# Kernel tuning notes

Hardware: AMD Instinct MI355X
Metric: run time of the kernel (lower is better)

Reference implementation:

```python
import jax, jax.numpy as jnp
import numpy as np

EPS = 1e-5

def layernorm(x, g, b):
    mu = jnp.mean(x, axis=-1, keepdims=True)
    var = jnp.mean(jnp.square(x - mu), axis=-1, keepdims=True)
    return (x - mu) * jax.lax.rsqrt(var + EPS) * g + b

def setup_inputs() -> dict:
    key = jax.random.key(0)
    B, T, C, H = 4, 2048, 1024, 16
    hs = C // H
    ks = jax.random.split(key, 16)
    s_in = 0.02
    return {
        "x": jax.random.normal(ks[0], (B, T, C), jnp.float32),
        "ln1_g": jnp.ones((C,), jnp.float32),
        "ln1_b": jnp.zeros((C,), jnp.float32),
        "Wq": jax.random.normal(ks[1], (H, C, hs), jnp.float32) * s_in,
        "Wk": jax.random.normal(ks[2], (H, C, hs), jnp.float32) * s_in,
        "Wv": jax.random.normal(ks[3], (H, C, hs), jnp.float32) * s_in,
        "Wo": jax.random.normal(ks[4], (C, C), jnp.float32) * s_in,
        "bo": jnp.zeros((C,), jnp.float32),
        "ln2_g": jnp.ones((C,), jnp.float32),
        "ln2_b": jnp.zeros((C,), jnp.float32),
        "W1": jax.random.normal(ks[5], (C, 4 * C), jnp.float32) * s_in,
        "b1": jnp.zeros((4 * C,), jnp.float32),
        "W2": jax.random.normal(ks[6], (4 * C, C), jnp.float32) * s_in,
        "b2": jnp.zeros((C,), jnp.float32),
    }

def reference(x, ln1_g, ln1_b, Wq, Wk, Wv, Wo, bo, ln2_g, ln2_b, W1, b1, W2, b2):
    B, T, C = x.shape
    H, _, hs = Wq.shape
    # --- multi-head causal self-attention on LN1(x) ---
    h = layernorm(x, ln1_g, ln1_b)
    q = jnp.einsum('btc,hcs->bhts', h, Wq)
    k = jnp.einsum('btc,hcs->bhts', h, Wk)
    v = jnp.einsum('btc,hcs->bhts', h, Wv)
    scores = jnp.einsum('bhqs,bhks->bhqk', q, k) * (hs ** -0.5)
    causal = jnp.tril(jnp.ones((T, T), bool))
    scores = jnp.where(causal, scores, -jnp.inf)
    attn = jax.nn.softmax(scores, axis=-1)  # dropout p=0 -> identity
    out = jnp.einsum('bhqk,bhks->bhqs', attn, v)
    out = out.transpose(0, 2, 1, 3).reshape(B, T, H * hs)  # concat heads
    x = x + out @ Wo + bo
    # --- feed-forward on LN2(x) ---
    h2 = layernorm(x, ln2_g, ln2_b)
    ff = jax.nn.relu(h2 @ W1 + b1) @ W2 + b2
    return x + ff
```

## Files before the change

### kernel.cpp

```cpp
#include <hip/hip_runtime.h>
#include <math.h>

#define B_  4
#define T_  2048
#define C_  1024
#define H_  16
#define HS_ 64
#define BT_ (B_*T_)
#define F_  (4*C_)
#define N3_ (3*C_)

typedef unsigned short ushort_t;
typedef __attribute__((ext_vector_type(4))) unsigned short us4;
typedef __attribute__((ext_vector_type(8))) unsigned short us8;
typedef __attribute__((ext_vector_type(4))) float f32x4;
typedef __attribute__((ext_vector_type(8))) __bf16 bf16x8;

template<bool V> struct bool_c { static constexpr bool value = V; };

__device__ __forceinline__ float bf2f(ushort_t u) {
    union { unsigned int i; float f; } c; c.i = ((unsigned int)u) << 16; return c.f;
}
__device__ __forceinline__ ushort_t f2bf(float f) {
    union { __bf16 b; ushort_t u; } c; c.b = (__bf16)f; return c.u;
}

#define GLB_(p) ((const __attribute__((address_space(1))) unsigned int*)(size_t)(p))
#define LDS_(p) ((__attribute__((address_space(3))) unsigned int*)(unsigned int)(size_t)(p))
__device__ __forceinline__ void gload16(const void* g, void* l) {
    __builtin_amdgcn_global_load_lds(GLB_(g), LDS_(l), 16, 0, 0);
}

template<int N> __device__ __forceinline__ void vm_wait() {
    if constexpr (N >= 8)      asm volatile("s_waitcnt vmcnt(8)" ::: "memory");
    else if constexpr (N == 6) asm volatile("s_waitcnt vmcnt(6)" ::: "memory");
    else if constexpr (N == 4) asm volatile("s_waitcnt vmcnt(4)" ::: "memory");
    else if constexpr (N == 3) asm volatile("s_waitcnt vmcnt(3)" ::: "memory");
    else if constexpr (N == 2) asm volatile("s_waitcnt vmcnt(2)" ::: "memory");
    else                       asm volatile("s_waitcnt vmcnt(0)" ::: "memory");
}

__global__ __launch_bounds__(256) void repack_qkv_k(
    const float* __restrict__ Wq, const float* __restrict__ Wk,
    const float* __restrict__ Wv, ushort_t* __restrict__ WtB)
{
    __shared__ float tile[64][65];
    int bid = blockIdx.x;
    int p  = bid >> 8;
    int h  = (bid >> 4) & 15;
    int c0 = (bid & 15) * 64;
    const float* W = (p == 0) ? Wq : ((p == 1) ? Wk : Wv);
    int t = threadIdx.x;
    int cl = t >> 2, seg = (t & 3) * 16;
    const float* src = W + ((size_t)h * C_ + c0 + cl) * HS_ + seg;
#pragma unroll
    for (int i = 0; i < 4; i++) {
        float4 v = *(const float4*)(src + i * 4);
        tile[cl][seg + i*4 + 0] = v.x; tile[cl][seg + i*4 + 1] = v.y;
        tile[cl][seg + i*4 + 2] = v.z; tile[cl][seg + i*4 + 3] = v.w;
    }
    __syncthreads();
    int sl = t >> 2;
    int n = p * C_ + h * HS_ + sl;
    ushort_t* dst = WtB + (size_t)n * C_ + c0 + seg;
    us8 o0, o1;
#pragma unroll
    for (int e = 0; e < 8; e++) { o0[e] = f2bf(tile[seg + e][sl]); o1[e] = f2bf(tile[seg + 8 + e][sl]); }
    *(us8*)dst = o0; *(us8*)(dst + 8) = o1;
}

__global__ __launch_bounds__(256) void transpose_k(
    const float* __restrict__ in, ushort_t* __restrict__ out, int K, int N)
{
    __shared__ float tile[64][65];
    int n0 = blockIdx.x * 64, k0 = blockIdx.y * 64;
    int t = threadIdx.x;
    int kl = t >> 2, seg = (t & 3) * 16;
    const float* src = in + (size_t)(k0 + kl) * N + n0 + seg;
#pragma unroll
    for (int i = 0; i < 4; i++) {
        float4 v = *(const float4*)(src + i * 4);
        tile[kl][seg + i*4 + 0] = v.x; tile[kl][seg + i*4 + 1] = v.y;
        tile[kl][seg + i*4 + 2] = v.z; tile[kl][seg + i*4 + 3] = v.w;
    }
    __syncthreads();
    int nl = t >> 2;
    ushort_t* dst = out + (size_t)(n0 + nl) * K + k0 + seg;
    us8 o0, o1;
#pragma unroll
    for (int e = 0; e < 8; e++) { o0[e] = f2bf(tile[seg + e][nl]); o1[e] = f2bf(tile[seg + 8 + e][nl]); }
    *(us8*)dst = o0; *(us8*)(dst + 8) = o1;
}

__global__ __launch_bounds__(256) void transv_k(
    const ushort_t* __restrict__ QKV, ushort_t* __restrict__ Vt)
{
    __shared__ ushort_t tl[64][72];
    int bid = blockIdx.x;
    int tt = bid & 31;
    int bh = bid >> 5;
    int b  = bh >> 4;
    int h  = bh & 15;
    int t = threadIdx.x;
    int r = t >> 2, sg = (t & 3) * 16;
    const ushort_t* src = QKV + (size_t)(b * T_ + tt * 64 + r) * N3_ + 2 * C_ + h * HS_ + sg;
    us8 a0 = *(const us8*)src;
    us8 a1 = *(const us8*)(src + 8);
#pragma unroll
    for (int e = 0; e < 8; e++) { tl[r][sg + e] = a0[e]; tl[r][sg + 8 + e] = a1[e]; }
    __syncthreads();
    ushort_t* dst = Vt + ((size_t)(b * H_ + h) * HS_ + r) * T_ + tt * 64 + sg;
    us8 o0, o1;
#pragma unroll
    for (int e = 0; e < 8; e++) { o0[e] = tl[sg + e][r]; o1[e] = tl[sg + 8 + e][r]; }
    *(us8*)dst = o0; *(us8*)(dst + 8) = o1;
}

template<int IN_BF16>
__global__ __launch_bounds__(256) void ln_k(
    const void* __restrict__ xv, const float* __restrict__ g,
    const float* __restrict__ b, ushort_t* __restrict__ out)
{
    int row = blockIdx.x;
    int t = threadIdx.x;
    float v[4];
    if (IN_BF16) {
        const ushort_t* xr = (const ushort_t*)xv + (size_t)row * C_;
        us4 u = *(const us4*)(xr + t * 4);
#pragma unroll
        for (int i = 0; i < 4; i++) v[i] = bf2f(u[i]);
    } else {
        const float* xr = (const float*)xv + (size_t)row * C_;
        float4 f = *(const float4*)(xr + t * 4);
        v[0] = f.x; v[1] = f.y; v[2] = f.z; v[3] = f.w;
    }
    float s  = v[0] + v[1] + v[2] + v[3];
    float ss = v[0]*v[0] + v[1]*v[1] + v[2]*v[2] + v[3]*v[3];
#pragma unroll
    for (int off = 32; off > 0; off >>= 1) {
        s  += __shfl_xor(s, off);
        ss += __shfl_xor(ss, off);
    }
    __shared__ float red[8];
    int wv = t >> 6;
    if ((t & 63) == 0) { red[wv*2] = s; red[wv*2+1] = ss; }
    __syncthreads();
    s  = red[0] + red[2] + red[4] + red[6];
    ss = red[1] + red[3] + red[5] + red[7];
    float mu  = s * (1.0f / C_);
    float var = ss * (1.0f / C_) - mu * mu;
    float rs  = rsqrtf(var + 1e-5f);
    float4 gv = *(const float4*)(g + t * 4);
    float4 bv = *(const float4*)(b + t * 4);
    us4 o;
    o[0] = f2bf((v[0] - mu) * rs * gv.x + bv.x);
    o[1] = f2bf((v[1] - mu) * rs * gv.y + bv.y);
    o[2] = f2bf((v[2] - mu) * rs * gv.z + bv.z);
    o[3] = f2bf((v[3] - mu) * rs * gv.w + bv.w);
    *(us4*)(out + (size_t)row * C_ + t * 4) = o;
}

template<int BM, int BN, int WM, int WN, int RELU, int BIAS, int RES_MODE, int OUT_BF16>
__global__ __launch_bounds__(WM * WN * 64) void mgemm8_k(
    const ushort_t* __restrict__ A, const ushort_t* __restrict__ Bw,
    const float* __restrict__ bias, const void* __restrict__ res,
    void* __restrict__ out, int M, int N, int K, int lda, int gx)
{
    constexpr int THREADS = WM * WN * 64;
    constexpr int MIa = BM / WM / 16;
    constexpr int MIb = BN / WN / 16;
    constexpr int A_INSTS = (BM * 64) / (16 * THREADS);
    constexpr int B_INSTS = (BN * 64) / (16 * THREADS);
    constexpr int UNIT = A_INSTS + B_INSTS;
    __shared__ ushort_t As[4 * BM * 32];
    __shared__ ushort_t Bs[4 * BN * 32];

    int tid = threadIdx.x;
    int l = tid & 63, w = tid >> 6;
    int wm = w / WN, wn = w % WN;
    int lin = blockIdx.x;
    int nwg = gridDim.x;
    int swz = (lin & 7) * (nwg >> 3) + (lin >> 3);
    int bx = swz % gx, by = swz / gx;
    int m0 = by * BM, n0 = bx * BN;
    const int nt = K >> 6;

    auto stageA = [&](int tile, int kh) {
        ushort_t* dst = As + ((tile & 1) * 2 + kh) * (BM * 32);
#pragma unroll
        for (int inst = 0; inst < A_INSTS; ++inst) {
            int slot = inst * THREADS + tid;
            int row = slot >> 2, q = slot & 3;
            const ushort_t* src = A + (size_t)(m0 + row) * lda + tile * 64 + kh * 32
                                  + ((q ^ ((row >> 1) & 3)) * 8);
            gload16(src, dst + (inst * THREADS + w * 64) * 8);
        }
    };
    auto stageB = [&](int tile, int kh) {
        ushort_t* dst = Bs + ((tile & 1) * 2 + kh) * (BN * 32);
#pragma unroll
        for (int inst = 0; inst < B_INSTS; ++inst) {
            int slot = inst * THREADS + tid;
            int row = slot >> 2, q = slot & 3;
            const ushort_t* src = Bw + (size_t)(n0 + row) * K + tile * 64 + kh * 32
                                  + ((q ^ ((row >> 1) & 3)) * 8);
            gload16(src, dst + (inst * THREADS + w * 64) * 8);
        }
    };

    f32x4 acc[MIa][MIb];
#pragma unroll
    for (int i = 0; i < MIa; i++)
#pragma unroll
        for (int j = 0; j < MIb; j++) acc[i][j] = (f32x4){0.f, 0.f, 0.f, 0.f};

    stageA(0, 0); stageB(0, 0);
    stageA(0, 1); stageB(0, 1);
    stageA(1, 0); stageB(1, 0);

    for (int t = 0; t < nt; ++t) {
        int buf = t & 1;
#pragma unroll
        for (int kh = 0; kh < 2; ++kh) {
            if (t == nt - 1) { if (kh == 0) vm_wait<UNIT>(); else vm_wait<0>(); }
            else vm_wait<2 * UNIT>();
            __builtin_amdgcn_s_barrier();
            __builtin_amdgcn_sched_barrier(0);

            const ushort_t* Ab = As + (buf * 2 + kh) * (BM * 32);
            const ushort_t* Bb = Bs + (buf * 2 + kh) * (BN * 32);
            bf16x8 af[MIa], bf[MIb];
#pragma unroll
            for (int i = 0; i < MIa; ++i) {
                int row = wm * (BM / WM) + i * 16 + (l & 15);
                af[i] = *(const bf16x8*)(Ab + row * 32 + (((l >> 4) ^ ((row >> 1) & 3)) * 8));
            }
#pragma unroll
            for (int j = 0; j < MIb; ++j) {
                int row = wn * (BN / WN) + j * 16 + (l & 15);
                bf[j] = *(const bf16x8*)(Bb + row * 32 + (((l >> 4) ^ ((row >> 1) & 3)) * 8));
            }
            if (kh == 0) { if (t + 1 < nt) { stageA(t + 1, 1); stageB(t + 1, 1); } }
            else         { if (t + 2 < nt) { stageA(t + 2, 0); stageB(t + 2, 0); } }

            __builtin_amdgcn_s_setprio(1);
#pragma unroll
            for (int i = 0; i < MIa; ++i)
#pragma unroll
                for (int j = 0; j < MIb; ++j)
                    acc[i][j] = __builtin_amdgcn_mfma_f32_16x16x32_bf16(af[i], bf[j], acc[i][j], 0, 0, 0);
            __builtin_amdgcn_s_setprio(0);
            __builtin_amdgcn_sched_barrier(0);
            __builtin_amdgcn_s_barrier();
        }
    }

    int colb = n0 + wn * (BN / WN) + (l & 15);
    int rowb = m0 + wm * (BM / WM) + ((l >> 4) << 2);
#pragma unroll
    for (int j = 0; j < MIb; j++) {
        int col = colb + j * 16;
        float bval = BIAS ? bias[col] : 0.f;
#pragma unroll
        for (int i = 0; i < MIa; i++) {
#pragma unroll
            for (int r = 0; r < 4; r++) {
                int row = rowb + i * 16 + r;
                float v = acc[i][j][r] + bval;
                if (RELU) v = fmaxf(v, 0.f);
                size_t idx = (size_t)row * N + col;
                if (RES_MODE == 1) v += ((const float*)res)[idx];
                else if (RES_MODE == 2) v += bf2f(((const ushort_t*)res)[idx]);
                if (OUT_BF16) ((ushort_t*)out)[idx] = f2bf(v);
                else          ((float*)out)[idx]    = v;
            }
        }
    }
}

__global__ __launch_bounds__(256) void fattn_k(
    ushort_t* __restrict__ QKV, const ushort_t* __restrict__ Vt)
{
    __shared__ ushort_t QPs[64 * 64];
    __shared__ ushort_t Ks[2][64 * 64];
    __shared__ ushort_t Vs[2][64 * 64];
    int lin = blockIdx.x;
    int nwg = gridDim.x;
    int bid = (lin & 7) * (nwg >> 3) + (lin >> 3);
    int pr = bid & 15;
    int bh = bid >> 4;
    int b  = bh >> 4;
    int h  = bh & 15;
    int tid = threadIdx.x;
    int lid = tid & 63, w = tid >> 6;

    int srow = w * 16 + (lid >> 3);
    int sseg0 = (lid & 7) ^ (srow & 7);
    int sseg1 = (lid & 7) ^ ((srow + 8) & 7);
    const ushort_t* Kg = QKV + (size_t)(b * T_) * N3_ + C_ + h * HS_;
    const ushort_t* Vg = Vt + (size_t)(b * H_ + h) * HS_ * T_;

    int mrow = w * 16 + (lid & 15);
    int fseg = lid >> 4;
    int qlocb = w * 16 + ((lid >> 4) << 2);

    const __bf16 oneb = (__bf16)1.0f;
    bf16x8 ones = {oneb, oneb, oneb, oneb, oneb, oneb, oneb, oneb};

    for (int half = 0; half < 2; ++half) {
        int qt = half ? (31 - pr) : pr;
        const ushort_t* Qg = QKV + (size_t)(b * T_ + qt * 64) * N3_ + h * HS_;

        gload16(Qg + (size_t)srow * N3_ + sseg0 * 8,       QPs + w * 1024);
        gload16(Qg + (size_t)(srow + 8) * N3_ + sseg1 * 8, QPs + w * 1024 + 512);
        gload16(Kg + (size_t)srow * N3_ + sseg0 * 8,       Ks[0] + w * 1024);
        gload16(Kg + (size_t)(srow + 8) * N3_ + sseg1 * 8, Ks[0] + w * 1024 + 512);
        gload16(Vg + (size_t)srow * T_ + sseg0 * 8,        Vs[0] + w * 1024);
        gload16(Vg + (size_t)(srow + 8) * T_ + sseg1 * 8,  Vs[0] + w * 1024 + 512);
        __syncthreads();

        bf16x8 aqr[2];
        aqr[0] = *(const bf16x8*)(QPs + mrow * 64 + (((0 + fseg) ^ (mrow & 7)) * 8));
        aqr[1] = *(const bf16x8*)(QPs + mrow * 64 + (((4 + fseg) ^ (mrow & 7)) * 8));

        f32x4 accO[4];
#pragma unroll
        for (int j = 0; j < 4; j++) accO[j] = (f32x4){0.f, 0.f, 0.f, 0.f};
        f32x4 accL = (f32x4){0.f, 0.f, 0.f, 0.f};

        auto body = [&](auto diag_c, int kt) {
            constexpr bool DIAG = decltype(diag_c)::value;
            int cur = kt & 1;
            if (!DIAG) {
                int nk = kt + 1;
                gload16(Kg + (size_t)(nk * 64 + srow) * N3_ + sseg0 * 8,     Ks[cur ^ 1] + w * 1024);
                gload16(Kg + (size_t)(nk * 64 + srow + 8) * N3_ + sseg1 * 8, Ks[cur ^ 1] + w * 1024 + 512);
                gload16(Vg + (size_t)srow * T_ + nk * 64 + sseg0 * 8,        Vs[cur ^ 1] + w * 1024);
                gload16(Vg + (size_t)(srow + 8) * T_ + nk * 64 + sseg1 * 8,  Vs[cur ^ 1] + w * 1024 + 512);
            }
            const ushort_t* Kc = Ks[cur];
            const ushort_t* Vc = Vs[cur];

            f32x4 s[4];
#pragma unroll
            for (int j = 0; j < 4; j++) s[j] = (f32x4){0.f, 0.f, 0.f, 0.f};
            __builtin_amdgcn_s_setprio(1);
#pragma unroll
            for (int ks = 0; ks < 2; ks++) {
#pragma unroll
                for (int j = 0; j < 4; j++) {
                    int krow = j * 16 + (lid & 15);
                    bf16x8 bk = *(const bf16x8*)(Kc + krow * 64 + (((ks * 4 + fseg) ^ (krow & 7)) * 8));
                    s[j] = __builtin_amdgcn_mfma_f32_16x16x32_bf16(aqr[ks], bk, s[j], 0, 0, 0);
                }
            }
            __builtin_amdgcn_s_setprio(0);

#pragma unroll
            for (int r = 0; r < 4; r++) {
                int qloc = qlocb + r;
#pragma unroll
                for (int j = 0; j < 4; j++) {
                    int col = j * 16 + (lid & 15);
                    float p = __expf(s[j][r] * 0.125f);
                    if (DIAG) { if (col > qloc) p = 0.f; }
                    QPs[qloc * 64 + (((col >> 3) ^ (qloc & 7)) * 8) + (col & 7)] = f2bf(p);
                }
            }

            __builtin_amdgcn_s_setprio(1);
#pragma unroll
            for (int ks = 0; ks < 2; ks++) {
                bf16x8 ap = *(const bf16x8*)(QPs + mrow * 64 + (((ks * 4 + fseg) ^ (mrow & 7)) * 8));
                accL = __builtin_amdgcn_mfma_f32_16x16x32_bf16(ap, ones, accL, 0, 0, 0);
#pragma unroll
                for (int j = 0; j < 4; j++) {
                    int drow = j * 16 + (lid & 15);
                    bf16x8 bv = *(const bf16x8*)(Vc + drow * 64 + (((ks * 4 + fseg) ^ (drow & 7)) * 8));
                    accO[j] = __builtin_amdgcn_mfma_f32_16x16x32_bf16(ap, bv, accO[j], 0, 0, 0);
                }
            }
            __builtin_amdgcn_s_setprio(0);
            __syncthreads();
        };

        for (int kt = 0; kt < qt; ++kt) body(bool_c<false>{}, kt);
        body(bool_c<true>{}, qt);

#pragma unroll
        for (int r = 0; r < 4; r++) {
            float inv = 1.0f / accL[r];
            int qabs = qt * 64 + qlocb + r;
            ushort_t* orow = QKV + (size_t)(b * T_ + qabs) * N3_ + h * HS_;
#pragma unroll
            for (int j = 0; j < 4; j++)
                orow[j * 16 + (lid & 15)] = f2bf(accO[j][r] * inv);
        }
    }
}

extern "C" void kernel_launch(void* const* d_in, const int* in_sizes, int n_in,
                              void* d_out, int out_size, void* d_ws, size_t ws_size,
                              hipStream_t stream)
{
    const float* x   = (const float*)d_in[0];
    const float* g1  = (const float*)d_in[1];
    const float* be1 = (const float*)d_in[2];
    const float* Wq  = (const float*)d_in[3];
    const float* Wk  = (const float*)d_in[4];
    const float* Wv  = (const float*)d_in[5];
    const float* Wo  = (const float*)d_in[6];
    const float* bo  = (const float*)d_in[7];
    const float* g2  = (const float*)d_in[8];
    const float* be2 = (const float*)d_in[9];
    const float* W1  = (const float*)d_in[10];
    const float* b1  = (const float*)d_in[11];
    const float* W2  = (const float*)d_in[12];
    const float* b2  = (const float*)d_in[13];

    const size_t UB2 = (size_t)BT_ * C_ * 2;
    const size_t WT_B = (size_t)N3_ * C_ * 2;
    const size_t WO_B = (size_t)C_ * C_ * 2;
    const size_t W1_B = (size_t)C_ * F_ * 2;
    const size_t REQ = 5 * UB2 + WT_B + WO_B + 2 * W1_B;
    if (ws_size < REQ) {
        hipMemsetAsync(d_out, 0, (size_t)out_size * 4, stream);
        return;
    }
    char* wsb = (char*)d_ws;
    ushort_t* hB   = (ushort_t*)(wsb);
    ushort_t* qkvB = (ushort_t*)(wsb + UB2);
    ushort_t* ff1B = qkvB;
    ushort_t* WtB  = (ushort_t*)(wsb + 5 * UB2);
    ushort_t* WoB  = (ushort_t*)(wsb + 5 * UB2 + WT_B);
    ushort_t* W1B  = (ushort_t*)(wsb + 5 * UB2 + WT_B + WO_B);
    ushort_t* W2B  = (ushort_t*)(wsb + 5 * UB2 + WT_B + WO_B + W1_B);
    float* x2F = (float*)d_out;

    repack_qkv_k<<<3 * 16 * 16, 256, 0, stream>>>(Wq, Wk, Wv, WtB);
    transpose_k<<<dim3(C_ / 64, C_ / 64), 256, 0, stream>>>(Wo, WoB, C_, C_);
    transpose_k<<<dim3(F_ / 64, C_ / 64), 256, 0, stream>>>(W1, W1B, C_, F_);
    transpose_k<<<dim3(C_ / 64, F_ / 64), 256, 0, stream>>>(W2, W2B, F_, C_);

    ln_k<0><<<BT_, 256, 0, stream>>>(x, g1, be1, hB);
    mgemm8_k<128,256,2,4,0,0,0,1><<<(N3_ / 256) * (BT_ / 128), 512, 0, stream>>>(
        hB, WtB, nullptr, nullptr, qkvB, BT_, N3_, C_, C_, N3_ / 256);
    transv_k<<<B_ * H_ * (T_ / 64), 256, 0, stream>>>(qkvB, hB);
    fattn_k<<<B_ * H_ * 16, 256, 0, stream>>>(qkvB, hB);
    mgemm8_k<128,256,2,4,0,1,1,0><<<(C_ / 256) * (BT_ / 128), 512, 0, stream>>>(
        qkvB, WoB, bo, x, x2F, BT_, C_, C_, N3_, C_ / 256);
    ln_k<0><<<BT_, 256, 0, stream>>>(x2F, g2, be2, hB);
    mgemm8_k<256,256,2,4,1,1,0,1><<<(F_ / 256) * (BT_ / 256), 512, 0, stream>>>(
        hB, W1B, b1, nullptr, ff1B, BT_, F_, C_, C_, F_ / 256);
    mgemm8_k<128,256,2,4,0,1,1,0><<<(C_ / 256) * (BT_ / 128), 512, 0, stream>>>(
        ff1B, W2B, b2, x2F, (float*)d_out, BT_, C_, F_, F_, C_ / 256);
}
```

Before: 364.0 us.

## Software-pipeline attention: compute next QK^T tile while doing softmax/PV of current

Restructures the flash-attention loop so the QK^T MFMAs for key tile kt+1 are issued before the exp/softmax and PV work of tile kt. K gets a triple buffer and is prefetched two tiles ahead, and V is prefetched one tile ahead. The goal is to overlap MFMA latency with the exp and LDS-store phase. In exchange it holds an extra score accumulator set in registers and adds 8KB of LDS, which may lower occupancy.

```diff
diff --git a/kernel.cpp b/kernel.cpp
--- a/kernel.cpp
+++ b/kernel.cpp
@@ -282,7 +282,7 @@
     ushort_t* __restrict__ QKV, const ushort_t* __restrict__ Vt)
 {
     __shared__ ushort_t QPs[64 * 64];
-    __shared__ ushort_t Ks[2][64 * 64];
+    __shared__ ushort_t Ks[3][64 * 64];
     __shared__ ushort_t Vs[2][64 * 64];
     int lin = blockIdx.x;
     int nwg = gridDim.x;
@@ -307,16 +307,26 @@
     const __bf16 oneb = (__bf16)1.0f;
     bf16x8 ones = {oneb, oneb, oneb, oneb, oneb, oneb, oneb, oneb};
 
+    auto stageK = [&](int kt) {
+        ushort_t* d = Ks[kt % 3];
+        gload16(Kg + (size_t)(kt * 64 + srow) * N3_ + sseg0 * 8,     d + w * 1024);
+        gload16(Kg + (size_t)(kt * 64 + srow + 8) * N3_ + sseg1 * 8, d + w * 1024 + 512);
+    };
+    auto stageV = [&](int kt) {
+        ushort_t* d = Vs[kt & 1];
+        gload16(Vg + (size_t)srow * T_ + kt * 64 + sseg0 * 8,       d + w * 1024);
+        gload16(Vg + (size_t)(srow + 8) * T_ + kt * 64 + sseg1 * 8, d + w * 1024 + 512);
+    };
+
     for (int half = 0; half < 2; ++half) {
         int qt = half ? (31 - pr) : pr;
         const ushort_t* Qg = QKV + (size_t)(b * T_ + qt * 64) * N3_ + h * HS_;
 
         gload16(Qg + (size_t)srow * N3_ + sseg0 * 8,       QPs + w * 1024);
         gload16(Qg + (size_t)(srow + 8) * N3_ + sseg1 * 8, QPs + w * 1024 + 512);
-        gload16(Kg + (size_t)srow * N3_ + sseg0 * 8,       Ks[0] + w * 1024);
-        gload16(Kg + (size_t)(srow + 8) * N3_ + sseg1 * 8, Ks[0] + w * 1024 + 512);
-        gload16(Vg + (size_t)srow * T_ + sseg0 * 8,        Vs[0] + w * 1024);
-        gload16(Vg + (size_t)(srow + 8) * T_ + sseg1 * 8,  Vs[0] + w * 1024 + 512);
+        stageK(0);
+        stageV(0);
+        if (qt >= 1) stageK(1);
         __syncthreads();
 
         bf16x8 aqr[2];
@@ -328,20 +338,7 @@
         for (int j = 0; j < 4; j++) accO[j] = (f32x4){0.f, 0.f, 0.f, 0.f};
         f32x4 accL = (f32x4){0.f, 0.f, 0.f, 0.f};
 
-        auto body = [&](auto diag_c, int kt) {
-            constexpr bool DIAG = decltype(diag_c)::value;
-            int cur = kt & 1;
-            if (!DIAG) {
-                int nk = kt + 1;
-                gload16(Kg + (size_t)(nk * 64 + srow) * N3_ + sseg0 * 8,     Ks[cur ^ 1] + w * 1024);
-                gload16(Kg + (size_t)(nk * 64 + srow + 8) * N3_ + sseg1 * 8, Ks[cur ^ 1] + w * 1024 + 512);
-                gload16(Vg + (size_t)srow * T_ + nk * 64 + sseg0 * 8,        Vs[cur ^ 1] + w * 1024);
-                gload16(Vg + (size_t)(srow + 8) * T_ + nk * 64 + sseg1 * 8,  Vs[cur ^ 1] + w * 1024 + 512);
-            }
-            const ushort_t* Kc = Ks[cur];
-            const ushort_t* Vc = Vs[cur];
-
-            f32x4 s[4];
+        auto qk_into = [&](const ushort_t* Kc, f32x4* s) {
 #pragma unroll
             for (int j = 0; j < 4; j++) s[j] = (f32x4){0.f, 0.f, 0.f, 0.f};
             __builtin_amdgcn_s_setprio(1);
@@ -355,7 +352,9 @@
                 }
             }
             __builtin_amdgcn_s_setprio(0);
-
+        };
+        auto smax_pv = [&](auto diag_c, f32x4* s, const ushort_t* Vc) {
+            constexpr bool DIAG = decltype(diag_c)::value;
 #pragma unroll
             for (int r = 0; r < 4; r++) {
                 int qloc = qlocb + r;
@@ -367,7 +366,6 @@
                     QPs[qloc * 64 + (((col >> 3) ^ (qloc & 7)) * 8) + (col & 7)] = f2bf(p);
                 }
             }
-
             __builtin_amdgcn_s_setprio(1);
 #pragma unroll
             for (int ks = 0; ks < 2; ks++) {
@@ -381,11 +379,22 @@
                 }
             }
             __builtin_amdgcn_s_setprio(0);
+        };
+
+        f32x4 sP[4], sN[4];
+        qk_into(Ks[0], sP);
+
+        for (int kt = 0; kt < qt; ++kt) {
+            if (kt + 2 <= qt) stageK(kt + 2);
+            stageV(kt + 1);
+            qk_into(Ks[(kt + 1) % 3], sN);
+            smax_pv(bool_c<false>{}, sP, Vs[kt & 1]);
             __syncthreads();
-        };
-
-        for (int kt = 0; kt < qt; ++kt) body(bool_c<false>{}, kt);
-        body(bool_c<true>{}, qt);
+#pragma unroll
+            for (int j = 0; j < 4; j++) sP[j] = sN[j];
+        }
+        smax_pv(bool_c<true>{}, sP, Vs[qt & 1]);
+        __syncthreads();
 
 #pragma unroll
         for (int r = 0; r < 4; r++) {
```

After: 361.2 us, median of 2. No clear change (-0.8%).
